# Performance work log

Hardware: AMD Instinct MI355X
Metric: run time of the kernel (lower is better)

## Reference

```python
import jax, jax.numpy as jnp
import numpy as np

H, W, T = 720, 1280, 20
B, N = 8, 500000


def setup_inputs() -> dict:
    key = jax.random.key(0)
    kx, ky, kt, kp, kc = jax.random.split(key, 5)
    x = jnp.floor(jax.random.uniform(kx, (B, N)) * W)          # pixel x in [0, W)
    y = jnp.floor(jax.random.uniform(ky, (B, N)) * H)          # pixel y in [0, H)
    t = jax.random.uniform(kt, (B, N))                          # normalized time in [0, 1]
    p = jax.random.bernoulli(kp, 0.5, (B, N)).astype(jnp.float32)  # polarity {0,1}
    eventBlock = jnp.stack([x, y, t, p], axis=-1).astype(jnp.float32)  # (B, N, 4)
    eventCounts = jax.random.randint(kc, (B,), N // 2, N + 1).astype(jnp.int64)
    return {"eventBlock": eventBlock, "eventCounts": eventCounts}


def reference(eventBlock, eventCounts):
    # events -> (B, W, H, T) voxel grid via temporal bilinear scatter-add,
    # then permute(0,3,2,1) -> (B, T, H, W) as in EV2VoxelGrid.forward
    x = eventBlock[..., 0].astype(jnp.int32)                    # (B, N)
    y = eventBlock[..., 1].astype(jnp.int32)
    t = eventBlock[..., 2]
    pol = eventBlock[..., 3] * 2.0 - 1.0                        # {0,1} -> {-1,+1}

    valid = jnp.arange(N)[None, :] < eventCounts[:, None]       # (B, N) mask by counts

    tb = t * (T - 1)                                            # continuous bin coord
    k0 = jnp.floor(tb).astype(jnp.int32)
    w1 = tb - k0.astype(tb.dtype)
    w0 = 1.0 - w1
    k0c = jnp.clip(k0, 0, T - 1)
    k1c = jnp.clip(k0 + 1, 0, T - 1)

    xc = jnp.clip(x, 0, W - 1)
    yc = jnp.clip(y, 0, H - 1)
    b = jnp.arange(B, dtype=jnp.int32)[:, None]                 # (B, 1)
    base = ((b * W + xc) * H + yc) * T                          # flat (b, x, y) offset

    v0 = jnp.where(valid, pol * w0, 0.0)
    v1 = jnp.where(valid, pol * w1, 0.0)

    grid = jnp.zeros((B * W * H * T,), dtype=eventBlock.dtype)
    grid = grid.at[(base + k0c).ravel()].add(v0.ravel())
    grid = grid.at[(base + k1c).ravel()].add(v1.ravel())
    grid = grid.reshape(B, W, H, T)
    return jnp.transpose(grid, (0, 3, 2, 1))                    # (B, T, H, W)
```

## Files before the change

### kernel.cpp

```cpp
#include <hip/hip_runtime.h>

#define GH 720
#define GW 1280
#define GT 20
#define GB 8
#define NEV 500000
#define TOTAL (GB * NEV)

#define CY 90
#define NCOARSE (GB * CY)
#define CAPC 6144
#define PAD 32
#define EVB 8192
#define NBLK1 ((TOTAL + EVB - 1) / EVB)

#define TY 8
#define TX 64
#define NTXB (GW / TX)
#define NFINE (NCOARSE * NTXB)
#define OVF_CAP (1u << 20)

typedef float vfloat4 __attribute__((ext_vector_type(4)));

__global__ __launch_bounds__(256) void k_zero(unsigned* __restrict__ gcnt)
{
    int i = blockIdx.x * blockDim.x + threadIdx.x;
    if (i < NCOARSE * PAD + 1) gcnt[i] = 0u;
}

__global__ __launch_bounds__(256) void k_part(
    const float4* __restrict__ ev, const int* __restrict__ counts,
    unsigned* __restrict__ gcnt, uint2* __restrict__ buckets,
    uint2* __restrict__ ovf)
{
    __shared__ unsigned hist[NCOARSE];
    __shared__ unsigned lbase[NCOARSE];
    __shared__ unsigned hist2[NCOARSE];
    const int tid = threadIdx.x;
    const int base = blockIdx.x * EVB + tid;

    for (int c = tid; c < NCOARSE; c += 256) { hist[c] = 0u; hist2[c] = 0u; }
    __syncthreads();

    for (int j = 0; j < EVB / 256; j++) {
        int i = base + j * 256;
        if (i >= TOTAL) break;
        int b = i / NEV;
        int n = i - b * NEV;
        if (n >= counts[b]) continue;
        float4 e = ev[i];
        int y = min(max((int)e.y, 0), GH - 1);
        atomicAdd(&hist[b * CY + (y >> 3)], 1u);
    }
    __syncthreads();

    for (int c = tid; c < NCOARSE; c += 256) {
        unsigned h = hist[c];
        lbase[c] = h ? atomicAdd(&gcnt[c * PAD], h) : 0u;
    }
    __syncthreads();

    for (int j = 0; j < EVB / 256; j++) {
        int i = base + j * 256;
        if (i >= TOTAL) break;
        int b = i / NEV;
        int n = i - b * NEV;
        if (n >= counts[b]) continue;
        float4 e = ev[i];
        int x = min(max((int)e.x, 0), GW - 1);
        int y = min(max((int)e.y, 0), GH - 1);
        int c = b * CY + (y >> 3);

        float tb = e.z * (float)(GT - 1);
        int k0 = (int)floorf(tb);
        float w1 = tb - (float)k0;
        int k0c = min(max(k0, 0), GT - 1);
        unsigned p = (e.w > 0.5f) ? 1u : 0u;

        unsigned word0 = (unsigned)x | ((unsigned)y << 11) | (p << 21)
                       | ((unsigned)k0c << 22) | ((unsigned)b << 27);
        uint2 rec = make_uint2(word0, __float_as_uint(w1));

        unsigned pos = lbase[c] + atomicAdd(&hist2[c], 1u);
        if (pos < CAPC) {
            buckets[(size_t)c * CAPC + pos] = rec;
        } else {
            unsigned o = atomicAdd(&gcnt[NCOARSE * PAD], 1u);
            if (o < OVF_CAP) ovf[o] = rec;
        }
    }
}

__global__ __launch_bounds__(256) void k_fine(
    const uint2* __restrict__ buckets, const unsigned* __restrict__ gcnt,
    unsigned* __restrict__ starts_f, unsigned* __restrict__ cnt_f,
    uint2* __restrict__ arr2)
{
    __shared__ uint2 stash[CAPC];
    __shared__ unsigned fhist[NTXB], foff[NTXB], fh2[NTXB];
    const int c = blockIdx.x;
    const int tid = threadIdx.x;
    if (tid < NTXB) { fhist[tid] = 0u; fh2[tid] = 0u; }
    __syncthreads();

    unsigned m = min(gcnt[c * PAD], (unsigned)CAPC);
    for (unsigned idx = tid; idx < m; idx += 256) {
        uint2 r = buckets[(size_t)c * CAPC + idx];
        stash[idx] = r;
        atomicAdd(&fhist[(r.x & 2047) >> 6], 1u);
    }
    __syncthreads();

    if (tid == 0) {
        unsigned s = 0;
        for (int t = 0; t < NTXB; t++) { foff[t] = s; s += fhist[t]; }
    }
    __syncthreads();

    if (tid < NTXB) {
        starts_f[c * NTXB + tid] = (unsigned)(c * CAPC) + foff[tid];
        cnt_f[c * NTXB + tid]    = fhist[tid];
    }
    for (unsigned idx = tid; idx < m; idx += 256) {
        uint2 r = stash[idx];
        unsigned tx = (r.x & 2047) >> 6;
        unsigned rk = atomicAdd(&fh2[tx], 1u);
        arr2[(size_t)c * CAPC + foff[tx] + rk] = r;
    }
}

__global__ __launch_bounds__(256) void k_accum(
    const uint2* __restrict__ arr2, const unsigned* __restrict__ starts_f,
    const unsigned* __restrict__ cnt_f, float* __restrict__ out)
{
    __shared__ float tile[GT * TY * TX];
    const int f = blockIdx.x;
    const int tid = threadIdx.x;

    vfloat4* t4z = (vfloat4*)tile;
    for (int j = tid; j < GT * TY * (TX / 4); j += 256) t4z[j] = (vfloat4){0.f, 0.f, 0.f, 0.f};
    __syncthreads();

    unsigned s = starts_f[f], m = cnt_f[f];
    for (unsigned idx = tid; idx < m; idx += 256) {
        uint2 r = arr2[s + idx];
        int x  = r.x & 2047;
        int y  = (r.x >> 11) & 1023;
        int p  = (r.x >> 21) & 1;
        int k0 = (r.x >> 22) & 31;
        float w1 = __uint_as_float(r.y);
        float w0 = 1.0f - w1;
        float pol = p ? 1.0f : -1.0f;
        int k1 = min(k0 + 1, GT - 1);
        int yy = y & (TY - 1);
        int xx = x & (TX - 1);
        atomicAdd(&tile[(k0 * TY + yy) * TX + xx], pol * w0);
        atomicAdd(&tile[(k1 * TY + yy) * TX + xx], pol * w1);
    }
    __syncthreads();

    int b   = f / (CY * NTXB);
    int rem = f % (CY * NTXB);
    int ty  = rem / NTXB;
    int tx  = rem % NTXB;
    int y0 = ty * TY;
    int x0 = tx * TX;

    const vfloat4* t4 = (const vfloat4*)tile;
    vfloat4* o4 = (vfloat4*)out;
    for (int j = tid; j < GT * TY * (TX / 4); j += 256) {
        int row = j >> 4;
        int col = j & 15;
        int k  = row >> 3;
        int yy = row & (TY - 1);
        int off = ((b * GT + k) * GH + (y0 + yy)) * (GW / 4) + (x0 >> 2) + col;
        __builtin_nontemporal_store(t4[j], &o4[off]);
    }
}

__global__ __launch_bounds__(256) void k_overflow(
    const uint2* __restrict__ ovf, const unsigned* __restrict__ gcnt,
    float* __restrict__ out)
{
    unsigned n = min(gcnt[NCOARSE * PAD], OVF_CAP);
    for (unsigned i = blockIdx.x * blockDim.x + threadIdx.x; i < n;
         i += gridDim.x * blockDim.x) {
        uint2 r = ovf[i];
        int x  = r.x & 2047;
        int y  = (r.x >> 11) & 1023;
        int p  = (r.x >> 21) & 1;
        int k0 = (r.x >> 22) & 31;
        int b  = (r.x >> 27) & 7;
        float w1 = __uint_as_float(r.y);
        float w0 = 1.0f - w1;
        float pol = p ? 1.0f : -1.0f;
        int k1 = min(k0 + 1, GT - 1);
        atomicAdd(&out[((b * GT + k0) * GH + y) * GW + x], pol * w0);
        atomicAdd(&out[((b * GT + k1) * GH + y) * GW + x], pol * w1);
    }
}

__global__ __launch_bounds__(256) void ev2voxel_scatter(
    const float4* __restrict__ ev, const int* __restrict__ counts,
    float* __restrict__ out)
{
    int i = blockIdx.x * blockDim.x + threadIdx.x;
    if (i >= TOTAL) return;
    int b = i / NEV;
    int n = i - b * NEV;
    if (n >= counts[b]) return;
    float4 e = ev[i];
    int x = min(max((int)e.x, 0), GW - 1);
    int y = min(max((int)e.y, 0), GH - 1);
    float pol = e.w * 2.0f - 1.0f;
    float tb = e.z * (float)(GT - 1);
    int k0 = (int)floorf(tb);
    float w1 = tb - (float)k0;
    float w0 = 1.0f - w1;
    int k0c = min(max(k0, 0), GT - 1);
    int k1c = min(max(k0 + 1, 0), GT - 1);
    int rowbase = (b * GT) * GH;
    atomicAdd(&out[(rowbase + k0c * GH + y) * GW + x], pol * w0);
    atomicAdd(&out[(rowbase + k1c * GH + y) * GW + x], pol * w1);
}

extern "C" void kernel_launch(void* const* d_in, const int* in_sizes, int n_in,
                              void* d_out, int out_size, void* d_ws, size_t ws_size,
                              hipStream_t stream) {
    const float4* ev = (const float4*)d_in[0];
    const int* counts = (const int*)d_in[1];
    float* out = (float*)d_out;

    const size_t gcnt_off   = 0;
    const size_t starts_off = (size_t)NCOARSE * PAD + PAD;
    const size_t cntf_off   = starts_off + NFINE;
    size_t bucket_off       = cntf_off + NFINE;
    if (bucket_off & 1) bucket_off++;
    const size_t arr2_off = bucket_off + (size_t)NCOARSE * CAPC * 2;
    const size_t ovf_off  = arr2_off + (size_t)NCOARSE * CAPC * 2;
    const size_t need_bytes = (ovf_off + (size_t)OVF_CAP * 2) * 4;

    if (ws_size < need_bytes) {
        (void)hipMemsetAsync(out, 0, (size_t)out_size * sizeof(float), stream);
        ev2voxel_scatter<<<(TOTAL + 255) / 256, 256, 0, stream>>>(ev, counts, out);
        return;
    }

    unsigned* ws = (unsigned*)d_ws;
    unsigned* gcnt     = ws + gcnt_off;
    unsigned* starts_f = ws + starts_off;
    unsigned* cnt_f    = ws + cntf_off;
    uint2* buckets = (uint2*)(ws + bucket_off);
    uint2* arr2    = (uint2*)(ws + arr2_off);
    uint2* ovf     = (uint2*)(ws + ovf_off);

    k_zero<<<(NCOARSE * PAD + 1 + 255) / 256, 256, 0, stream>>>(gcnt);
    k_part<<<NBLK1, 256, 0, stream>>>(ev, counts, gcnt, buckets, ovf);
    k_fine<<<NCOARSE, 256, 0, stream>>>(buckets, gcnt, starts_f, cnt_f, arr2);
    k_accum<<<NFINE, 256, 0, stream>>>(arr2, starts_f, cnt_f, out);
    k_overflow<<<64, 256, 0, stream>>>(ovf, gcnt, out);
}
```

Before: 189.6 us.

## Fuse fine partition into accumulation and pack bucket records to 32 bits

```diff
diff --git a/kernel.cpp b/kernel.cpp
--- a/kernel.cpp
+++ b/kernel.cpp
@@ -17,10 +17,10 @@
 #define TY 8
 #define TX 64
 #define NTXB (GW / TX)
-#define NFINE (NCOARSE * NTXB)
 #define OVF_CAP (1u << 20)
 
 typedef float vfloat4 __attribute__((ext_vector_type(4)));
+
 
 __global__ __launch_bounds__(256) void k_zero(unsigned* __restrict__ gcnt)
 {
@@ -30,7 +30,7 @@
 
 __global__ __launch_bounds__(256) void k_part(
     const float4* __restrict__ ev, const int* __restrict__ counts,
-    unsigned* __restrict__ gcnt, uint2* __restrict__ buckets,
+    unsigned* __restrict__ gcnt, unsigned* __restrict__ buckets,
     uint2* __restrict__ ovf)
 {
     __shared__ unsigned hist[NCOARSE];
@@ -77,104 +77,68 @@
         int k0c = min(max(k0, 0), GT - 1);
         unsigned p = (e.w > 0.5f) ? 1u : 0u;
 
-        unsigned word0 = (unsigned)x | ((unsigned)y << 11) | (p << 21)
-                       | ((unsigned)k0c << 22) | ((unsigned)b << 27);
-        uint2 rec = make_uint2(word0, __float_as_uint(w1));
-
         unsigned pos = lbase[c] + atomicAdd(&hist2[c], 1u);
         if (pos < CAPC) {
+            unsigned w1q = __float2uint_rn(w1 * 4095.0f);
+            unsigned rec = (unsigned)x | ((unsigned)(y & 7) << 11) | (p << 14)
+                         | ((unsigned)k0c << 15) | (w1q << 20);
             buckets[(size_t)c * CAPC + pos] = rec;
         } else {
+            unsigned word0 = (unsigned)x | ((unsigned)y << 11) | (p << 21)
+                           | ((unsigned)k0c << 22) | ((unsigned)b << 27);
             unsigned o = atomicAdd(&gcnt[NCOARSE * PAD], 1u);
-            if (o < OVF_CAP) ovf[o] = rec;
+            if (o < OVF_CAP) ovf[o] = make_uint2(word0, __float_as_uint(w1));
         }
     }
 }
 
-__global__ __launch_bounds__(256) void k_fine(
-    const uint2* __restrict__ buckets, const unsigned* __restrict__ gcnt,
-    unsigned* __restrict__ starts_f, unsigned* __restrict__ cnt_f,
-    uint2* __restrict__ arr2)
-{
-    __shared__ uint2 stash[CAPC];
-    __shared__ unsigned fhist[NTXB], foff[NTXB], fh2[NTXB];
+__global__ __launch_bounds__(256) void k_faccum(
+    const unsigned* __restrict__ buckets, const unsigned* __restrict__ gcnt,
+    float* __restrict__ out)
+{
+    __shared__ unsigned stash[CAPC];
+    __shared__ float tile[GT * TY * TX];
     const int c = blockIdx.x;
     const int tid = threadIdx.x;
-    if (tid < NTXB) { fhist[tid] = 0u; fh2[tid] = 0u; }
-    __syncthreads();
 
     unsigned m = min(gcnt[c * PAD], (unsigned)CAPC);
-    for (unsigned idx = tid; idx < m; idx += 256) {
-        uint2 r = buckets[(size_t)c * CAPC + idx];
-        stash[idx] = r;
-        atomicAdd(&fhist[(r.x & 2047) >> 6], 1u);
-    }
-    __syncthreads();
-
-    if (tid == 0) {
-        unsigned s = 0;
-        for (int t = 0; t < NTXB; t++) { foff[t] = s; s += fhist[t]; }
-    }
-    __syncthreads();
-
-    if (tid < NTXB) {
-        starts_f[c * NTXB + tid] = (unsigned)(c * CAPC) + foff[tid];
-        cnt_f[c * NTXB + tid]    = fhist[tid];
-    }
-    for (unsigned idx = tid; idx < m; idx += 256) {
-        uint2 r = stash[idx];
-        unsigned tx = (r.x & 2047) >> 6;
-        unsigned rk = atomicAdd(&fh2[tx], 1u);
-        arr2[(size_t)c * CAPC + foff[tx] + rk] = r;
-    }
-}
-
-__global__ __launch_bounds__(256) void k_accum(
-    const uint2* __restrict__ arr2, const unsigned* __restrict__ starts_f,
-    const unsigned* __restrict__ cnt_f, float* __restrict__ out)
-{
-    __shared__ float tile[GT * TY * TX];
-    const int f = blockIdx.x;
-    const int tid = threadIdx.x;
-
-    vfloat4* t4z = (vfloat4*)tile;
-    for (int j = tid; j < GT * TY * (TX / 4); j += 256) t4z[j] = (vfloat4){0.f, 0.f, 0.f, 0.f};
-    __syncthreads();
-
-    unsigned s = starts_f[f], m = cnt_f[f];
-    for (unsigned idx = tid; idx < m; idx += 256) {
-        uint2 r = arr2[s + idx];
-        int x  = r.x & 2047;
-        int y  = (r.x >> 11) & 1023;
-        int p  = (r.x >> 21) & 1;
-        int k0 = (r.x >> 22) & 31;
-        float w1 = __uint_as_float(r.y);
-        float w0 = 1.0f - w1;
-        float pol = p ? 1.0f : -1.0f;
-        int k1 = min(k0 + 1, GT - 1);
-        int yy = y & (TY - 1);
-        int xx = x & (TX - 1);
-        atomicAdd(&tile[(k0 * TY + yy) * TX + xx], pol * w0);
-        atomicAdd(&tile[(k1 * TY + yy) * TX + xx], pol * w1);
-    }
-    __syncthreads();
-
-    int b   = f / (CY * NTXB);
-    int rem = f % (CY * NTXB);
-    int ty  = rem / NTXB;
-    int tx  = rem % NTXB;
-    int y0 = ty * TY;
-    int x0 = tx * TX;
-
-    const vfloat4* t4 = (const vfloat4*)tile;
+    for (unsigned i = tid; i < m; i += 256)
+        stash[i] = buckets[(size_t)c * CAPC + i];
+    __syncthreads();
+
+    const int b  = c / CY;
+    const int y0 = (c % CY) * TY;
+    vfloat4* t4 = (vfloat4*)tile;
     vfloat4* o4 = (vfloat4*)out;
-    for (int j = tid; j < GT * TY * (TX / 4); j += 256) {
-        int row = j >> 4;
-        int col = j & 15;
-        int k  = row >> 3;
-        int yy = row & (TY - 1);
-        int off = ((b * GT + k) * GH + (y0 + yy)) * (GW / 4) + (x0 >> 2) + col;
-        __builtin_nontemporal_store(t4[j], &o4[off]);
+
+    for (int tx = 0; tx < NTXB; tx++) {
+        for (int j = tid; j < GT * TY * (TX / 4); j += 256)
+            t4[j] = (vfloat4){0.f, 0.f, 0.f, 0.f};
+        __syncthreads();
+
+        for (unsigned idx = tid; idx < m; idx += 256) {
+            unsigned r = stash[idx];
+            if ((int)((r & 2047u) >> 6) != tx) continue;
+            int xx = r & 63;
+            int yy = (r >> 11) & 7;
+            float pol = ((r >> 14) & 1u) ? 1.0f : -1.0f;
+            int k0 = (r >> 15) & 31;
+            float w1 = (float)(r >> 20) * (1.0f / 4095.0f);
+            int k1 = min(k0 + 1, GT - 1);
+            atomicAdd(&tile[(k0 * TY + yy) * TX + xx], pol * (1.0f - w1));
+            atomicAdd(&tile[(k1 * TY + yy) * TX + xx], pol * w1);
+        }
+        __syncthreads();
+
+        for (int j = tid; j < GT * TY * (TX / 4); j += 256) {
+            int row = j >> 4;
+            int col = j & 15;
+            int k  = row >> 3;
+            int yy = row & 7;
+            int off = ((b * GT + k) * GH + (y0 + yy)) * (GW / 4) + tx * (TX / 4) + col;
+            __builtin_nontemporal_store(t4[j], &o4[off]);
+        }
+        __syncthreads();
     }
 }
 
@@ -232,12 +196,9 @@
     float* out = (float*)d_out;
 
     const size_t gcnt_off   = 0;
-    const size_t starts_off = (size_t)NCOARSE * PAD + PAD;
-    const size_t cntf_off   = starts_off + NFINE;
-    size_t bucket_off       = cntf_off + NFINE;
-    if (bucket_off & 1) bucket_off++;
-    const size_t arr2_off = bucket_off + (size_t)NCOARSE * CAPC * 2;
-    const size_t ovf_off  = arr2_off + (size_t)NCOARSE * CAPC * 2;
+    const size_t bucket_off = (size_t)NCOARSE * PAD + PAD;
+    size_t ovf_off          = bucket_off + (size_t)NCOARSE * CAPC;
+    if (ovf_off & 1) ovf_off++;
     const size_t need_bytes = (ovf_off + (size_t)OVF_CAP * 2) * 4;
 
     if (ws_size < need_bytes) {
@@ -247,16 +208,12 @@
     }
 
     unsigned* ws = (unsigned*)d_ws;
-    unsigned* gcnt     = ws + gcnt_off;
-    unsigned* starts_f = ws + starts_off;
-    unsigned* cnt_f    = ws + cntf_off;
-    uint2* buckets = (uint2*)(ws + bucket_off);
-    uint2* arr2    = (uint2*)(ws + arr2_off);
-    uint2* ovf     = (uint2*)(ws + ovf_off);
+    unsigned* gcnt    = ws + gcnt_off;
+    unsigned* buckets = ws + bucket_off;
+    uint2*    ovf     = (uint2*)(ws + ovf_off);
 
     k_zero<<<(NCOARSE * PAD + 1 + 255) / 256, 256, 0, stream>>>(gcnt);
     k_part<<<NBLK1, 256, 0, stream>>>(ev, counts, gcnt, buckets, ovf);
-    k_fine<<<NCOARSE, 256, 0, stream>>>(buckets, gcnt, starts_f, cnt_f, arr2);
-    k_accum<<<NFINE, 256, 0, stream>>>(arr2, starts_f, cnt_f, out);
+    k_faccum<<<NCOARSE, 256, 0, stream>>>(buckets, gcnt, out);
     k_overflow<<<64, 256, 0, stream>>>(ovf, gcnt, out);
 }
```

Measured after the change: 220.8 us. +16.5%, slower.
